# Optimization experiments

Measured on AMD Instinct MI355X. Metric: run time of the kernel, lower is better.

Reference implementation:

```python
import jax, jax.numpy as jnp
import numpy as np

HIDDEN = 768
ENT = 9
D = 64  # inner_dim
BIG = 1e12


def _rope_tables(seq_len, dim):
    # layout after torch stack([sin,cos],-1).reshape: [sin0,cos0,sin1,cos1,...]
    pos = jnp.arange(seq_len, dtype=jnp.float32)[:, None]          # [S,1]
    inv = jnp.power(10000.0, -2.0 * jnp.arange(dim // 2, dtype=jnp.float32) / dim)
    ang = pos * inv                                                 # [S,D/2]
    # repeat_interleave(2): [c0,c0,c1,c1,...]
    cos = jnp.repeat(jnp.cos(ang), 2, axis=-1)[:, None, :]          # [S,1,D]
    sin = jnp.repeat(jnp.sin(ang), 2, axis=-1)[:, None, :]
    return sin, cos


def _rotate_half_interleaved(x):
    # stack([-x_odd, x_even], -1).reshape -> [-x1, x0, -x3, x2, ...]
    return jnp.stack([-x[..., 1::2], x[..., ::2]], axis=-1).reshape(x.shape)


def _multilabel_ce(logits, labels):
    # standard GlobalPointer multilabel categorical crossentropy
    B = logits.shape[0]
    y_pred = logits.reshape(B * ENT, -1)
    y_true = labels.reshape(B * ENT, -1)
    y_pred = (1.0 - 2.0 * y_true) * y_pred
    y_neg = y_pred - y_true * BIG
    y_pos = y_pred - (1.0 - y_true) * BIG
    neg = jnp.logaddexp(0.0, jax.scipy.special.logsumexp(y_neg, axis=-1))
    pos = jnp.logaddexp(0.0, jax.scipy.special.logsumexp(y_pos, axis=-1))
    return jnp.mean(neg + pos)


def setup_inputs() -> dict:
    key = jax.random.key(0)
    k1, k2, k3, k4 = jax.random.split(key, 4)
    B, S = 16, 512
    last_hidden_state = jax.random.normal(k1, (B, S, HIDDEN), dtype=jnp.float32)
    attention_mask = jnp.ones((B, S), dtype=jnp.int32)
    batch_labels = jax.random.randint(k2, (B, ENT, S, S), 0, 2).astype(jnp.int32)
    W = jax.random.normal(k3, (HIDDEN, ENT * D * 2), dtype=jnp.float32) * 0.02
    b = jnp.zeros((ENT * D * 2,), dtype=jnp.float32)
    return {"last_hidden_state": last_hidden_state, "attention_mask": attention_mask,
            "batch_labels": batch_labels, "W": W, "b": b}


def reference(last_hidden_state, attention_mask, batch_labels, W, b):
    B, S, _ = last_hidden_state.shape
    out = last_hidden_state @ W + b                     # [B,S,ENT*2D]
    out = out.reshape(B, S, ENT, 2 * D)
    qw, kw = out[..., :D], out[..., D:]                 # [B,S,ENT,D]

    sin, cos = _rope_tables(S, D)                       # [S,1,D]
    qw = qw * cos + _rotate_half_interleaved(qw) * sin
    kw = kw * cos + _rotate_half_interleaved(kw) * sin

    logits = jnp.einsum('bmhd,bnhd->bhmn', qw, kw)      # [B,ENT,S,S]

    pad = attention_mask.astype(jnp.float32)[:, None, None, :]  # mask over key dim n
    logits = logits * pad - (1.0 - pad) * BIG
    tril = jnp.tril(jnp.ones((S, S), dtype=jnp.float32), -1)
    logits = logits - tril * BIG
    temp_logits = logits / (D ** 0.5)

    loss = _multilabel_ce(temp_logits, batch_labels.astype(jnp.float32))
    return loss, temp_logits
```

## Files before the change

kernel.cpp:

```cpp
#include <hip/hip_runtime.h>
#include <hip/hip_bf16.h>

#define HID 768
#define ENTS 9
#define DD 64
#define NOUT 1152
#define BATCH 16
#define SEQ 512
#define BIGF 1000000000000.0f
#define BIG8 125000000000.0f
#define NCHUNK 16

typedef __attribute__((ext_vector_type(8))) short short8;
typedef __attribute__((ext_vector_type(4))) short short4_t;
typedef __attribute__((ext_vector_type(4))) float floatx4;
typedef __attribute__((ext_vector_type(2))) float floatx2;
typedef __attribute__((ext_vector_type(4))) int intx4;
typedef unsigned short ushort_t;

static __device__ __forceinline__ ushort_t f2bf(float x) {
    unsigned int u = __float_as_uint(x);
    unsigned int r = (u + 0x7FFFu + ((u >> 16) & 1u)) >> 16;
    return (ushort_t)r;
}

static __device__ __forceinline__ void gload16(const void* g, void* l) {
    __builtin_amdgcn_global_load_lds(
        (const __attribute__((address_space(1))) void*)g,
        (__attribute__((address_space(3))) void*)l, 16, 0, 0);
}

__global__ void rope_table_kernel(float* __restrict__ sin_t, float* __restrict__ cos_t) {
    int idx = blockIdx.x * blockDim.x + threadIdx.x;
    if (idx >= SEQ * 32) return;
    int m = idx >> 5, i = idx & 31;
    float inv = powf(10000.0f, -2.0f * (float)i / 64.0f);
    float ang = (float)m * inv;
    sin_t[idx] = sinf(ang);
    cos_t[idx] = cosf(ang);
}

__global__ void cvt_x_kernel(const float* __restrict__ X, ushort_t* __restrict__ Xb, int n) {
    int i = (blockIdx.x * blockDim.x + threadIdx.x) * 4;
    int stride = gridDim.x * blockDim.x * 4;
    for (; i < n; i += stride) {
        float4 f = *(const float4*)&X[i];
        ushort_t u0 = f2bf(f.x), u1 = f2bf(f.y), u2 = f2bf(f.z), u3 = f2bf(f.w);
        ushort_t* p = &Xb[i];
        p[0] = u0; p[1] = u1; p[2] = u2; p[3] = u3;
    }
}

__global__ void cvt_w_kernel(const float* __restrict__ W, ushort_t* __restrict__ Wt) {
    int idx = blockIdx.x * blockDim.x + threadIdx.x;
    if (idx >= NOUT * HID) return;
    int n = idx / HID, k = idx - n * HID;
    Wt[idx] = f2bf(W[(size_t)k * NOUT + n]);
}

__global__ __launch_bounds__(256) void proj_rope_kernel(
    const ushort_t* __restrict__ Xb, const ushort_t* __restrict__ Wt,
    const float* __restrict__ bias,
    const float* __restrict__ sin_t, const float* __restrict__ cos_t,
    ushort_t* __restrict__ qbuf, ushort_t* __restrict__ kbuf)
{
    __shared__ ushort_t As[128 * 32];
    __shared__ ushort_t Bs[128 * 32];
    const int tid  = threadIdx.x;
    const int lane = tid & 63;
    const int wave = tid >> 6;
    const int bm = blockIdx.x * 128;
    const int bn = blockIdx.y * 128;
    const int wm = (wave >> 1) * 64;
    const int wn = (wave & 1) * 64;

    floatx4 acc[4][4];
    #pragma unroll
    for (int j = 0; j < 4; ++j)
        #pragma unroll
        for (int i = 0; i < 4; ++i) { floatx4 z = {0.f,0.f,0.f,0.f}; acc[j][i] = z; }

    const int c0 = wave * 64 + lane;
    const int c1 = 256 + wave * 64 + lane;
    const int r0 = c0 >> 2, q0 = (c0 & 3) * 8;
    const int r1 = c1 >> 2, q1 = (c1 & 3) * 8;
    ushort_t* ldsA0 = As + wave * 512;
    ushort_t* ldsA1 = As + 2048 + wave * 512;
    ushort_t* ldsB0 = Bs + wave * 512;
    ushort_t* ldsB1 = Bs + 2048 + wave * 512;

    const int ko = (lane >> 4) * 8;
    const int lr = lane & 15;

    for (int kt = 0; kt < HID; kt += 32) {
        gload16(&Xb[(size_t)(bm + r0) * HID + kt + q0], ldsA0);
        gload16(&Xb[(size_t)(bm + r1) * HID + kt + q1], ldsA1);
        gload16(&Wt[(size_t)(bn + r0) * HID + kt + q0], ldsB0);
        gload16(&Wt[(size_t)(bn + r1) * HID + kt + q1], ldsB1);
        __syncthreads();

        short8 a[4], b[4];
        #pragma unroll
        for (int i = 0; i < 4; ++i) a[i] = *(const short8*)&As[(wm + i*16 + lr) * 32 + ko];
        #pragma unroll
        for (int j = 0; j < 4; ++j) b[j] = *(const short8*)&Bs[(wn + j*16 + lr) * 32 + ko];
        #pragma unroll
        for (int j = 0; j < 4; ++j)
            #pragma unroll
            for (int i = 0; i < 4; ++i)
                acc[j][i] = __builtin_amdgcn_mfma_f32_16x16x32_bf16(b[j], a[i], acc[j][i], 0, 0, 0);
        __syncthreads();
    }

    #pragma unroll
    for (int j = 0; j < 4; ++j) {
        const int n0 = bn + wn + j*16 + (lane >> 4) * 4;
        const int e   = n0 >> 7;
        const int dd0 = n0 & 127;
        const bool isq = dd0 < DD;
        const int d0  = isq ? dd0 : dd0 - DD;
        const float4 bv = *(const float4*)&bias[n0];
        #pragma unroll
        for (int i = 0; i < 4; ++i) {
            const int m = bm + wm + i*16 + lr;
            const int s  = m & (SEQ - 1);
            const int bb = m >> 9;
            const float c0f = cos_t[s*32 + (d0 >> 1)];
            const float s0f = sin_t[s*32 + (d0 >> 1)];
            const float c1f = cos_t[s*32 + (d0 >> 1) + 1];
            const float s1f = sin_t[s*32 + (d0 >> 1) + 1];
            const float v0 = acc[j][i][0] + bv.x;
            const float v1 = acc[j][i][1] + bv.y;
            const float v2 = acc[j][i][2] + bv.z;
            const float v3 = acc[j][i][3] + bv.w;
            const float o0 = v0 * c0f - v1 * s0f;
            const float o1 = v1 * c0f + v0 * s0f;
            const float o2 = v2 * c1f - v3 * s1f;
            const float o3 = v3 * c1f + v2 * s1f;
            short4_t sv = { (short)f2bf(o0), (short)f2bf(o1), (short)f2bf(o2), (short)f2bf(o3) };
            size_t oidx = (((size_t)(bb * ENTS + e) * SEQ) + s) * DD + d0;
            *(short4_t*)&(isq ? qbuf : kbuf)[oidx] = sv;
        }
    }
}

__global__ __launch_bounds__(256) void qk_mask_ce_kernel(
    const ushort_t* __restrict__ qbuf, const ushort_t* __restrict__ kbuf,
    const int* __restrict__ amask, const int* __restrict__ labels,
    float* __restrict__ logits, float* __restrict__ partials)
{
    __shared__ ushort_t Qs[128][72];
    __shared__ ushort_t Ks[128][72];
    __shared__ float ssn[4], ssp[4];
    const int tid  = threadIdx.x;
    const int lane = tid & 63;
    const int wave = tid >> 6;
    const int bm = blockIdx.x * 128;
    const int bn = blockIdx.y * 128;
    const int bh = blockIdx.z;
    const int b  = bh / ENTS;
    const int wm = (wave >> 1) * 64;
    const int wn = (wave & 1) * 64;
    const size_t base = (size_t)bh * SEQ * DD;

    const int g  = lane >> 4;
    const int lr = lane & 15;
    const int ko = g * 8;
    const int r0 = bm + wm + lr;
    const int W  = bn + wn;
    const int n00 = W + (g << 2);
    const int bhbase = bh << 18;

    const bool diag = (blockIdx.x == blockIdx.y);
    const float lowAdj = (blockIdx.x > blockIdx.y) ? -BIG8 : 0.0f;

    intx4 y[4][4];
    #pragma unroll
    for (int j = 0; j < 4; ++j)
        #pragma unroll
        for (int i = 0; i < 4; ++i)
            y[j][i] = __builtin_nontemporal_load(
                (const intx4*)&labels[bhbase + ((r0 + i*16) << 9) + n00 + j*16]);

    floatx4 pm8[4], pc[4];
    #pragma unroll
    for (int j = 0; j < 4; ++j) {
        const intx4 p4 = *(const intx4*)&amask[(b << 9) + n00 + j*16];
        #pragma unroll
        for (int rg = 0; rg < 4; ++rg) {
            const float pf = (float)p4[rg];
            pm8[j][rg] = pf * 0.125f;
            pc[j][rg]  = (pf - 1.0f) * BIG8 + lowAdj;
        }
    }

    {
        const int r  = tid >> 1;
        const int ks = (tid & 1) * 32;
        const ushort_t* gq = &qbuf[base + (size_t)(bm + r) * DD + ks];
        const ushort_t* gk = &kbuf[base + (size_t)(bn + r) * DD + ks];
        #pragma unroll
        for (int u = 0; u < 4; ++u) {
            *(short8*)&Qs[r][ks + u*8] = *(const short8*)(gq + u*8);
            *(short8*)&Ks[r][ks + u*8] = *(const short8*)(gk + u*8);
        }
    }
    __syncthreads();

    short8 a[2][4];
    #pragma unroll
    for (int kk = 0; kk < 2; ++kk)
        #pragma unroll
        for (int i = 0; i < 4; ++i)
            a[kk][i] = *(const short8*)&Qs[wm + i*16 + lr][kk*32 + ko];

    float smn = 0.f, smp = 0.f;
    float tl[4];
    float* __restrict__ lgb = logits + bhbase;

    #pragma unroll
    for (int jp = 0; jp < 2; ++jp) {
        const int jA = jp * 2, jB = jp * 2 + 1;

        floatx4 accA[4], accB[4];
        #pragma unroll
        for (int i = 0; i < 4; ++i) { floatx4 z = {0.f,0.f,0.f,0.f}; accA[i] = z; accB[i] = z; }
        #pragma unroll
        for (int kk = 0; kk < 2; ++kk) {
            const short8 bfA = *(const short8*)&Ks[wn + jA*16 + lr][kk*32 + ko];
            const short8 bfB = *(const short8*)&Ks[wn + jB*16 + lr][kk*32 + ko];
            #pragma unroll
            for (int i = 0; i < 4; ++i) {
                accA[i] = __builtin_amdgcn_mfma_f32_16x16x32_bf16(bfA, a[kk][i], accA[i], 0, 0, 0);
                accB[i] = __builtin_amdgcn_mfma_f32_16x16x32_bf16(bfB, a[kk][i], accB[i], 0, 0, 0);
            }
        }

        #pragma unroll
        for (int half = 0; half < 2; ++half) {
            const int j = half ? jB : jA;
            const floatx4 pm = pm8[j], pcj = pc[j];
            const int n0j = W + j*16 + (g << 2);
            #pragma unroll
            for (int i = 0; i < 4; ++i) {
                const int m = r0 + i*16;
                const int d = m - n0j;
                floatx4 v = half ? accB[i] : accA[i];
                const intx4 yv = y[j][i];
                #pragma unroll
                for (int rg = 0; rg < 4; ++rg) {
                    float t = fmaf(v[rg], pm[rg], pcj[rg]);
                    if (diag && (d > rg)) t -= BIG8;
                    v[rg] = t;
                    const int yy = yv[rg] & 1;
                    const float u = __uint_as_float(__float_as_uint(t) ^ ((unsigned)yy << 31));
                    const float cN = yy ? -BIGF : 0.0f;
                    const float cP = yy ? -BIG8 : -BIGF;
                    smn += __expf(u + cN);
                    smp += __expf(u + cP);
                }
                if (half) accB[i] = v; else accA[i] = v;
            }
        }

        #pragma unroll
        for (int i = 0; i < 4; ++i) {
            const floatx4 vA = accA[i], vB = accB[i];
            const int m = r0 + i*16;
            float* __restrict__ row = lgb + (m << 9);
            const float sameA  = __shfl(vA.w, (lane - 16) & 63);
            const float tailA  = __shfl(tl[i], lr + 48);
            const float sameB  = __shfl(vB.w, (lane - 16) & 63);
            const float crossB = __shfl(vA.w, lr + 48);
            const float uA0 = (g == 0) ? tailA  : sameA;
            const float uB0 = (g == 0) ? crossB : sameB;
            if (jp == 0 && g == 0) {
                row[W] = vA.x;
                floatx2 h2 = { vA.y, vA.z };
                *(floatx2*)&row[W + 1] = h2;
            } else {
                floatx4 uA = { uA0, vA.x, vA.y, vA.z };
                *(floatx4*)&row[W + jA*16 + (g << 2) - 1] = uA;
            }
            floatx4 uB = { uB0, vB.x, vB.y, vB.z };
            *(floatx4*)&row[W + jB*16 + (g << 2) - 1] = uB;
            tl[i] = vB.w;
        }
    }

    if (g == 3) {
        #pragma unroll
        for (int i = 0; i < 4; ++i) {
            const int m = r0 + i*16;
            lgb[(m << 9) + W + 63] = tl[i];
        }
    }

    #pragma unroll
    for (int off = 32; off > 0; off >>= 1) {
        smn += __shfl_down(smn, off);
        smp += __shfl_down(smp, off);
    }
    if (lane == 0) { ssn[wave] = smn; ssp[wave] = smp; }
    __syncthreads();
    if (tid == 0) {
        float SN = ssn[0] + ssn[1] + ssn[2] + ssn[3];
        float SP = ssp[0] + ssp[1] + ssp[2] + ssp[3];
        const int chunk = blockIdx.x * 4 + blockIdx.y;
        floatx2 res = { SN, SP };
        *(floatx2*)&partials[(size_t)(bh * NCHUNK + chunk) * 2] = res;
    }
}

static __device__ __forceinline__ float lae0(float x) {
    return fmaxf(x, 0.f) + log1pf(__expf(-fabsf(x)));
}

__global__ __launch_bounds__(256) void ce_final_kernel(
    const float* __restrict__ partials, float* __restrict__ out)
{
    __shared__ float red[256];
    const int t = threadIdx.x;
    float val = 0.f;
    if (t < BATCH * ENTS) {
        float SN = 0.f, SP = 0.f;
        for (int c = 0; c < NCHUNK; ++c) {
            SN += partials[(size_t)(t * NCHUNK + c) * 2];
            SP += partials[(size_t)(t * NCHUNK + c) * 2 + 1];
        }
        const float neg = log1pf(SN);
        const float pos = lae0(BIG8 + logf(SP));
        val = neg + pos;
    }
    red[t] = val;
    __syncthreads();
    for (int s2 = 128; s2 > 0; s2 >>= 1) {
        if (t < s2) red[t] += red[t + s2];
        __syncthreads();
    }
    if (t == 0) out[0] = red[0] / (float)(BATCH * ENTS);
}

extern "C" void kernel_launch(void* const* d_in, const int* in_sizes, int n_in,
                              void* d_out, int out_size, void* d_ws, size_t ws_size,
                              hipStream_t stream) {
    const float* X      = (const float*)d_in[0];
    const int*   amask  = (const int*)d_in[1];
    const int*   labels = (const int*)d_in[2];
    const float* W      = (const float*)d_in[3];
    const float* bias   = (const float*)d_in[4];

    float* out    = (float*)d_out;
    float* logits = out + 1;

    float* sin_t = (float*)d_ws;
    float* cos_t = sin_t + SEQ * 32;
    ushort_t* Xb   = (ushort_t*)(cos_t + SEQ * 32);
    ushort_t* Wt   = Xb + (size_t)BATCH * SEQ * HID;
    ushort_t* qbuf = Wt + (size_t)NOUT * HID;
    ushort_t* kbuf = qbuf + (size_t)BATCH * ENTS * SEQ * DD;
    float* partials = (float*)(kbuf + (size_t)BATCH * ENTS * SEQ * DD);

    rope_table_kernel<<<64, 256, 0, stream>>>(sin_t, cos_t);
    cvt_x_kernel<<<1024, 256, 0, stream>>>(X, Xb, BATCH * SEQ * HID);
    cvt_w_kernel<<<(NOUT * HID + 255) / 256, 256, 0, stream>>>(W, Wt);
    proj_rope_kernel<<<dim3(64, 9), 256, 0, stream>>>(Xb, Wt, bias, sin_t, cos_t, qbuf, kbuf);
    qk_mask_ce_kernel<<<dim3(4, 4, 144), 256, 0, stream>>>(qbuf, kbuf, amask, labels, logits, partials);
    ce_final_kernel<<<1, 256, 0, stream>>>(partials, out);
}
```

Before: 154.6 us.

## Fuse prep kernels, enlarge projection tile, remap qk grid, use nontemporal stores

Merges the rope-table, X conversion and W transpose kernels into one grid-stride prep kernel, which saves launches. Enlarges the projection GEMM tile to 256x128, with each wave covering 64 rows across all 128 columns, so each B fragment is reused more. Flattens the qk grid with a swizzled mapping so consecutive blocks spread across batch-heads, and writes the large logits output with nontemporal stores to avoid polluting the cache. The bigger tile raises accumulator register pressure and halves the projection grid, which may lower occupancy.

```diff
diff --git a/kernel.cpp b/kernel.cpp
--- a/kernel.cpp
+++ b/kernel.cpp
@@ -30,32 +30,31 @@
         (__attribute__((address_space(3))) void*)l, 16, 0, 0);
 }
 
-__global__ void rope_table_kernel(float* __restrict__ sin_t, float* __restrict__ cos_t) {
-    int idx = blockIdx.x * blockDim.x + threadIdx.x;
-    if (idx >= SEQ * 32) return;
-    int m = idx >> 5, i = idx & 31;
-    float inv = powf(10000.0f, -2.0f * (float)i / 64.0f);
-    float ang = (float)m * inv;
-    sin_t[idx] = sinf(ang);
-    cos_t[idx] = cosf(ang);
-}
-
-__global__ void cvt_x_kernel(const float* __restrict__ X, ushort_t* __restrict__ Xb, int n) {
-    int i = (blockIdx.x * blockDim.x + threadIdx.x) * 4;
-    int stride = gridDim.x * blockDim.x * 4;
-    for (; i < n; i += stride) {
-        float4 f = *(const float4*)&X[i];
-        ushort_t u0 = f2bf(f.x), u1 = f2bf(f.y), u2 = f2bf(f.z), u3 = f2bf(f.w);
-        ushort_t* p = &Xb[i];
-        p[0] = u0; p[1] = u1; p[2] = u2; p[3] = u3;
-    }
-}
-
-__global__ void cvt_w_kernel(const float* __restrict__ W, ushort_t* __restrict__ Wt) {
-    int idx = blockIdx.x * blockDim.x + threadIdx.x;
-    if (idx >= NOUT * HID) return;
-    int n = idx / HID, k = idx - n * HID;
-    Wt[idx] = f2bf(W[(size_t)k * NOUT + n]);
+__global__ __launch_bounds__(256) void prep_kernel(
+    const float* __restrict__ X, const float* __restrict__ W,
+    float* __restrict__ sin_t, float* __restrict__ cos_t,
+    ushort_t* __restrict__ Xb, ushort_t* __restrict__ Wt)
+{
+    const int tid = blockIdx.x * 256 + threadIdx.x;
+    const int nth = gridDim.x * 256;
+
+    for (int idx = tid; idx < SEQ * 32; idx += nth) {
+        int m = idx >> 5, i = idx & 31;
+        float inv = powf(10000.0f, -2.0f * (float)i / 64.0f);
+        float ang = (float)m * inv;
+        sin_t[idx] = sinf(ang);
+        cos_t[idx] = cosf(ang);
+    }
+    for (int idx = tid; idx < NOUT * HID; idx += nth) {
+        int n = idx / HID, k = idx - n * HID;
+        Wt[idx] = f2bf(W[(size_t)k * NOUT + n]);
+    }
+    const int nx4 = BATCH * SEQ * HID / 4;
+    for (int idx = tid; idx < nx4; idx += nth) {
+        float4 f = *(const float4*)&X[idx * 4];
+        ushort_t* p = &Xb[idx * 4];
+        p[0] = f2bf(f.x); p[1] = f2bf(f.y); p[2] = f2bf(f.z); p[3] = f2bf(f.w);
+    }
 }
 
 __global__ __launch_bounds__(256) void proj_rope_kernel(
@@ -64,65 +63,69 @@
     const float* __restrict__ sin_t, const float* __restrict__ cos_t,
     ushort_t* __restrict__ qbuf, ushort_t* __restrict__ kbuf)
 {
-    __shared__ ushort_t As[128 * 32];
+    __shared__ ushort_t As[256 * 32];
     __shared__ ushort_t Bs[128 * 32];
     const int tid  = threadIdx.x;
     const int lane = tid & 63;
     const int wave = tid >> 6;
-    const int bm = blockIdx.x * 128;
+    const int bm = blockIdx.x * 256;
     const int bn = blockIdx.y * 128;
-    const int wm = (wave >> 1) * 64;
-    const int wn = (wave & 1) * 64;
-
-    floatx4 acc[4][4];
-    #pragma unroll
-    for (int j = 0; j < 4; ++j)
+
+    floatx4 acc[8][4];
+    #pragma unroll
+    for (int j = 0; j < 8; ++j)
         #pragma unroll
         for (int i = 0; i < 4; ++i) { floatx4 z = {0.f,0.f,0.f,0.f}; acc[j][i] = z; }
 
-    const int c0 = wave * 64 + lane;
-    const int c1 = 256 + wave * 64 + lane;
-    const int r0 = c0 >> 2, q0 = (c0 & 3) * 8;
-    const int r1 = c1 >> 2, q1 = (c1 & 3) * 8;
-    ushort_t* ldsA0 = As + wave * 512;
-    ushort_t* ldsA1 = As + 2048 + wave * 512;
-    ushort_t* ldsB0 = Bs + wave * 512;
-    ushort_t* ldsB1 = Bs + 2048 + wave * 512;
-
-    const int ko = (lane >> 4) * 8;
+    const int g  = lane >> 4;
     const int lr = lane & 15;
+    const int ko = g * 8;
+
+    int rA[4], qA[4], rB[2], qB[2];
+    #pragma unroll
+    for (int u = 0; u < 4; ++u) { int c = u*256 + tid; rA[u] = c >> 2; qA[u] = (c & 3) * 8; }
+    #pragma unroll
+    for (int u = 0; u < 2; ++u) { int c = u*256 + tid; rB[u] = c >> 2; qB[u] = (c & 3) * 8; }
+    ushort_t* ldsA[4]; ushort_t* ldsB[2];
+    #pragma unroll
+    for (int u = 0; u < 4; ++u) ldsA[u] = As + (u*256 + wave*64) * 8;
+    #pragma unroll
+    for (int u = 0; u < 2; ++u) ldsB[u] = Bs + (u*256 + wave*64) * 8;
 
     for (int kt = 0; kt < HID; kt += 32) {
-        gload16(&Xb[(size_t)(bm + r0) * HID + kt + q0], ldsA0);
-        gload16(&Xb[(size_t)(bm + r1) * HID + kt + q1], ldsA1);
-        gload16(&Wt[(size_t)(bn + r0) * HID + kt + q0], ldsB0);
-        gload16(&Wt[(size_t)(bn + r1) * HID + kt + q1], ldsB1);
+        #pragma unroll
+        for (int u = 0; u < 4; ++u)
+            gload16(&Xb[(size_t)(bm + rA[u]) * HID + kt + qA[u]], ldsA[u]);
+        #pragma unroll
+        for (int u = 0; u < 2; ++u)
+            gload16(&Wt[(size_t)(bn + rB[u]) * HID + kt + qB[u]], ldsB[u]);
         __syncthreads();
 
-        short8 a[4], b[4];
-        #pragma unroll
-        for (int i = 0; i < 4; ++i) a[i] = *(const short8*)&As[(wm + i*16 + lr) * 32 + ko];
-        #pragma unroll
-        for (int j = 0; j < 4; ++j) b[j] = *(const short8*)&Bs[(wn + j*16 + lr) * 32 + ko];
-        #pragma unroll
-        for (int j = 0; j < 4; ++j)
+        short8 a[4];
+        #pragma unroll
+        for (int i = 0; i < 4; ++i)
+            a[i] = *(const short8*)&As[(wave*64 + i*16 + lr) * 32 + ko];
+        #pragma unroll
+        for (int j = 0; j < 8; ++j) {
+            const short8 b = *(const short8*)&Bs[(j*16 + lr) * 32 + ko];
             #pragma unroll
             for (int i = 0; i < 4; ++i)
-                acc[j][i] = __builtin_amdgcn_mfma_f32_16x16x32_bf16(b[j], a[i], acc[j][i], 0, 0, 0);
+                acc[j][i] = __builtin_amdgcn_mfma_f32_16x16x32_bf16(b, a[i], acc[j][i], 0, 0, 0);
+        }
         __syncthreads();
     }
 
-    #pragma unroll
-    for (int j = 0; j < 4; ++j) {
-        const int n0 = bn + wn + j*16 + (lane >> 4) * 4;
-        const int e   = n0 >> 7;
+    const int e = blockIdx.y;
+    #pragma unroll
+    for (int j = 0; j < 8; ++j) {
+        const int n0  = bn + j*16 + (g << 2);
         const int dd0 = n0 & 127;
         const bool isq = dd0 < DD;
         const int d0  = isq ? dd0 : dd0 - DD;
         const float4 bv = *(const float4*)&bias[n0];
         #pragma unroll
         for (int i = 0; i < 4; ++i) {
-            const int m = bm + wm + i*16 + lr;
+            const int m = bm + wave*64 + i*16 + lr;
             const int s  = m & (SEQ - 1);
             const int bb = m >> 9;
             const float c0f = cos_t[s*32 + (d0 >> 1)];
@@ -155,9 +158,13 @@
     const int tid  = threadIdx.x;
     const int lane = tid & 63;
     const int wave = tid >> 6;
-    const int bm = blockIdx.x * 128;
-    const int bn = blockIdx.y * 128;
-    const int bh = blockIdx.z;
+
+    const int wrk = (blockIdx.x & 7) * 288 + (blockIdx.x >> 3);
+    const int bh  = wrk >> 4;
+    const int xy  = wrk & 15;
+    const int bx  = xy >> 2, by = xy & 3;
+    const int bm = bx * 128;
+    const int bn = by * 128;
     const int b  = bh / ENTS;
     const int wm = (wave >> 1) * 64;
     const int wn = (wave & 1) * 64;
@@ -171,8 +178,8 @@
     const int n00 = W + (g << 2);
     const int bhbase = bh << 18;
 
-    const bool diag = (blockIdx.x == blockIdx.y);
-    const float lowAdj = (blockIdx.x > blockIdx.y) ? -BIG8 : 0.0f;
+    const bool diag = (bx == by);
+    const float lowAdj = (bx > by) ? -BIG8 : 0.0f;
 
     intx4 y[4][4];
     #pragma unroll
@@ -275,15 +282,15 @@
             const float uA0 = (g == 0) ? tailA  : sameA;
             const float uB0 = (g == 0) ? crossB : sameB;
             if (jp == 0 && g == 0) {
-                row[W] = vA.x;
+                __builtin_nontemporal_store(vA.x, &row[W]);
                 floatx2 h2 = { vA.y, vA.z };
-                *(floatx2*)&row[W + 1] = h2;
+                __builtin_nontemporal_store(h2, (floatx2*)&row[W + 1]);
             } else {
                 floatx4 uA = { uA0, vA.x, vA.y, vA.z };
-                *(floatx4*)&row[W + jA*16 + (g << 2) - 1] = uA;
+                __builtin_nontemporal_store(uA, (floatx4*)&row[W + jA*16 + (g << 2) - 1]);
             }
             floatx4 uB = { uB0, vB.x, vB.y, vB.z };
-            *(floatx4*)&row[W + jB*16 + (g << 2) - 1] = uB;
+            __builtin_nontemporal_store(uB, (floatx4*)&row[W + jB*16 + (g << 2) - 1]);
             tl[i] = vB.w;
         }
     }
@@ -292,7 +299,7 @@
         #pragma unroll
         for (int i = 0; i < 4; ++i) {
             const int m = r0 + i*16;
-            lgb[(m << 9) + W + 63] = tl[i];
+            __builtin_nontemporal_store(tl[i], &lgb[(m << 9) + W + 63]);
         }
     }
 
@@ -306,9 +313,8 @@
     if (tid == 0) {
         float SN = ssn[0] + ssn[1] + ssn[2] + ssn[3];
         float SP = ssp[0] + ssp[1] + ssp[2] + ssp[3];
-        const int chunk = blockIdx.x * 4 + blockIdx.y;
         floatx2 res = { SN, SP };
-        *(floatx2*)&partials[(size_t)(bh * NCHUNK + chunk) * 2] = res;
+        *(floatx2*)&partials[(size_t)(bh * NCHUNK + xy) * 2] = res;
     }
 }
 
@@ -361,10 +367,8 @@
     ushort_t* kbuf = qbuf + (size_t)BATCH * ENTS * SEQ * DD;
     float* partials = (float*)(kbuf + (size_t)BATCH * ENTS * SEQ * DD);
 
-    rope_table_kernel<<<64, 256, 0, stream>>>(sin_t, cos_t);
-    cvt_x_kernel<<<1024, 256, 0, stream>>>(X, Xb, BATCH * SEQ * HID);
-    cvt_w_kernel<<<(NOUT * HID + 255) / 256, 256, 0, stream>>>(W, Wt);
-    proj_rope_kernel<<<dim3(64, 9), 256, 0, stream>>>(Xb, Wt, bias, sin_t, cos_t, qbuf, kbuf);
-    qk_mask_ce_kernel<<<dim3(4, 4, 144), 256, 0, stream>>>(qbuf, kbuf, amask, labels, logits, partials);
+    prep_kernel<<<2048, 256, 0, stream>>>(X, W, sin_t, cos_t, Xb, Wt);
+    proj_rope_kernel<<<dim3(32, 9), 256, 0, stream>>>(Xb, Wt, bias, sin_t, cos_t, qbuf, kbuf);
+    qk_mask_ce_kernel<<<2304, 256, 0, stream>>>(qbuf, kbuf, amask, labels, logits, partials);
     ce_final_kernel<<<1, 256, 0, stream>>>(partials, out);
 }
```

Result: slower. 237.6 us (+53.7%).
